# Optimization experiments

Measured on AMD Instinct MI355X. Metric: run time of the kernel, lower is better.

Reference implementation:

```python
import jax, jax.numpy as jnp
import numpy as np

N = 10000      # nodes
E = 160000     # edges (before self-loops)
IN = 256       # input feature dim
H = 8          # heads
C1, C2, C3 = 64, 128, 256  # per-head out channels per layer
NEG_SLOPE = 0.2


def setup_inputs() -> dict:
    key = jax.random.key(0)
    ks = jax.random.split(key, 16)
    def glorot(k, shape):
        fan_in = shape[-1]
        return jax.random.normal(k, shape, dtype=jnp.float32) * (1.0 / np.sqrt(fan_in))
    x = jax.random.normal(ks[0], (N, IN), dtype=jnp.float32)
    edge_index = jax.random.randint(ks[1], (2, E), 0, N)
    # layer 1: in=IN, out=64 per head, concat
    W1  = glorot(ks[2], (H * C1, IN))
    as1 = glorot(ks[3], (H, C1)); ad1 = glorot(ks[4], (H, C1))
    b1  = jnp.zeros((H * C1,), jnp.float32)
    # layer 2: in=H*C1, out=128 per head, concat
    W2  = glorot(ks[5], (H * C2, H * C1))
    as2 = glorot(ks[6], (H, C2)); ad2 = glorot(ks[7], (H, C2))
    b2  = jnp.zeros((H * C2,), jnp.float32)
    # layer 3: in=H*C2, out=256 per head, mean over heads
    W3  = glorot(ks[8], (H * C3, H * C2))
    as3 = glorot(ks[9], (H, C3)); ad3 = glorot(ks[10], (H, C3))
    b3  = jnp.zeros((C3,), jnp.float32)
    return {"x": x, "edge_index": edge_index,
            "W1": W1, "as1": as1, "ad1": ad1, "b1": b1,
            "W2": W2, "as2": as2, "ad2": ad2, "b2": b2,
            "W3": W3, "as3": as3, "ad3": ad3, "b3": b3}


def gat_layer(x, src, dst, W, a_src, a_dst, b, concat, num_nodes):
    """PyG-style GATConv (inference, dropout off, self-loops already in src/dst)."""
    heads, c = a_src.shape
    h = (x @ W.T).reshape(num_nodes, heads, c)          # [N,H,C]
    alpha_src = (h * a_src).sum(-1)                      # [N,H]
    alpha_dst = (h * a_dst).sum(-1)                      # [N,H]
    e = jax.nn.leaky_relu(alpha_src[src] + alpha_dst[dst], NEG_SLOPE)  # [E,H]
    # segment softmax over edges grouped by destination node
    m = jax.ops.segment_max(e, dst, num_segments=num_nodes)
    m = jnp.where(jnp.isfinite(m), m, 0.0)
    p = jnp.exp(e - m[dst])                              # [E,H]
    s = jax.ops.segment_sum(p, dst, num_segments=num_nodes)
    alpha = p / (s[dst] + 1e-16)                         # [E,H]
    out = jax.ops.segment_sum(alpha[:, :, None] * h[src], dst,
                              num_segments=num_nodes)    # [N,H,C]
    out = out.reshape(num_nodes, heads * c) if concat else out.mean(axis=1)
    return out + b


def reference(x, edge_index, W1, as1, ad1, b1, W2, as2, ad2, b2, W3, as3, ad3, b3):
    n = x.shape[0]
    loop = jnp.arange(n, dtype=edge_index.dtype)         # add_self_loops=True
    src = jnp.concatenate([edge_index[0], loop])
    dst = jnp.concatenate([edge_index[1], loop])
    h = jax.nn.elu(gat_layer(x, src, dst, W1, as1, ad1, b1, True, n))
    h = jax.nn.elu(gat_layer(h, src, dst, W2, as2, ad2, b2, True, n))
    return gat_layer(h, src, dst, W3, as3, ad3, b3, False, n)
```

## Files before the change

kernel.cpp:

```cpp
#include <hip/hip_runtime.h>
#include <cstdint>

#define NNODES 10000
#define NEDGES 160000
#define TOT_E  (NEDGES + NNODES)
#define HEADS  8

typedef unsigned short u16;
typedef __attribute__((ext_vector_type(8))) _Float16 h8;
typedef __attribute__((ext_vector_type(4))) _Float16 h4;
typedef __attribute__((ext_vector_type(4))) float f4;

__device__ inline u16 f2h(float x) {
    union { _Float16 h; u16 u; } c; c.h = (_Float16)x; return c.u;
}

__device__ inline void gld16(const u16* g, u16* l) {
    __builtin_amdgcn_global_load_lds(
        (const __attribute__((address_space(1))) void*)g,
        (__attribute__((address_space(3))) void*)l, 16, 0, 0);
}

__global__ void count_k(const int* __restrict__ ei, int* __restrict__ deg) {
    int i = blockIdx.x * 256 + threadIdx.x;
    if (i >= TOT_E) return;
    int dst = (i < NEDGES) ? ei[NEDGES + i] : (i - NEDGES);
    atomicAdd(deg + dst, 1);
}

__global__ __launch_bounds__(1024) void scan_k(const int* __restrict__ deg,
                                               int* __restrict__ rows) {
    __shared__ int buf[1024];
    int tid = threadIdx.x;
    int base = tid * 10;
    int loc[10]; int s = 0;
    #pragma unroll
    for (int j = 0; j < 10; j++) {
        int i = base + j;
        loc[j] = s;
        s += (i < NNODES) ? deg[i] : 0;
    }
    buf[tid] = s;
    __syncthreads();
    for (int off = 1; off < 1024; off <<= 1) {
        int t = (tid >= off) ? buf[tid - off] : 0;
        __syncthreads();
        buf[tid] += t;
        __syncthreads();
    }
    int ex = tid ? buf[tid - 1] : 0;
    #pragma unroll
    for (int j = 0; j < 10; j++) {
        int i = base + j;
        if (i < NNODES) rows[i] = ex + loc[j];
    }
    if (tid == 1023) rows[NNODES] = buf[1023];
}

__global__ void scatter_k(const int* __restrict__ ei, const int* __restrict__ rows,
                          int* __restrict__ cursor, int* __restrict__ esrc) {
    int i = blockIdx.x * 256 + threadIdx.x;
    if (i >= TOT_E) return;
    int src, dst;
    if (i < NEDGES) { src = ei[i]; dst = ei[NEDGES + i]; }
    else            { src = i - NEDGES; dst = src; }
    int pos = atomicAdd(cursor + dst, 1);
    esrc[rows[dst] + pos] = src;
}

__global__ void cvt16_k(const float* __restrict__ in, u16* __restrict__ o, int n4) {
    int i = blockIdx.x * 256 + threadIdx.x;
    if (i >= n4) return;
    float4 v = ((const float4*)in)[i];
    ushort4 h;
    h.x = f2h(v.x); h.y = f2h(v.y); h.z = f2h(v.z); h.w = f2h(v.w);
    ((ushort4*)o)[i] = h;
}

__global__ __launch_bounds__(256) void gemm_f16(
    const u16* __restrict__ A, const u16* __restrict__ B,
    u16* __restrict__ C16, int M, int N, int K,
    const float* __restrict__ a_s, const float* __restrict__ a_d,
    float* __restrict__ asrc, float* __restrict__ adst, int Chead)
{
    __shared__ u16 sA[4096], sB[4096];
    const int t = threadIdx.x, lane = t & 63, w = t >> 6;
    const int row0 = blockIdx.y * 128, col0 = blockIdx.x * 128;
    const int wm = w & 1, wn = w >> 1;
    const int l15 = lane & 15, quad = lane >> 4;

    const int octg = (lane & 3) ^ ((lane >> 3) & 3);
    const int rl   = lane >> 2;
    const u16* gp[4]; u16* lp[4];
    #pragma unroll
    for (int q = 0; q < 4; q++) {
        int c = w * 4 + q;
        if (c < 8) {
            int gr = row0 + c * 16 + rl; if (gr >= M) gr = M - 1;
            gp[q] = A + (size_t)gr * K + octg * 8;
            lp[q] = sA + c * 512;
        } else {
            int gc = col0 + (c - 8) * 16 + rl;
            gp[q] = B + (size_t)gc * K + octg * 8;
            lp[q] = sB + (c - 8) * 512;
        }
    }

    const int sw   = (l15 >> 1) & 3;
    const int aoff = (wm * 64 + l15) * 32 + ((quad ^ sw) * 8);
    const int boff = (wn * 64 + l15) * 32 + ((quad ^ sw) * 8);

    f4 acc[4][4];
    #pragma unroll
    for (int i = 0; i < 4; i++)
        #pragma unroll
        for (int j = 0; j < 4; j++)
            acc[i][j] = (f4){0.f, 0.f, 0.f, 0.f};

    for (int k0 = 0; k0 < K; k0 += 32) {
        #pragma unroll
        for (int q = 0; q < 4; q++) {
            gld16(gp[q], lp[q]);
            gp[q] += 32;
        }
        __syncthreads();

        h8 a[4];
        #pragma unroll
        for (int i = 0; i < 4; i++)
            a[i] = *(const h8*)&sA[aoff + i * 512];
        #pragma unroll
        for (int j = 0; j < 4; j++) {
            h8 b = *(const h8*)&sB[boff + j * 512];
            #pragma unroll
            for (int i = 0; i < 4; i++)
                acc[i][j] = __builtin_amdgcn_mfma_f32_16x16x32_f16(a[i], b, acc[i][j], 0, 0, 0);
        }
        __syncthreads();
    }

    const int span0 = col0 + wn * 64;
    const int hd = span0 / Chead;
    float av[4], dv[4];
    #pragma unroll
    for (int j = 0; j < 4; j++) {
        av[j] = a_s[span0 + j * 16 + l15];
        dv[j] = a_d[span0 + j * 16 + l15];
    }

    #pragma unroll
    for (int i = 0; i < 4; i++) {
        #pragma unroll
        for (int r = 0; r < 4; r++) {
            int gr = row0 + wm * 64 + i * 16 + quad * 4 + r;
            float s1 = 0.f, s2 = 0.f;
            #pragma unroll
            for (int j = 0; j < 4; j++) {
                float v = acc[i][j][r];
                s1 += v * av[j];
                s2 += v * dv[j];
            }
            #pragma unroll
            for (int m = 1; m < 16; m <<= 1) {
                s1 += __shfl_xor(s1, m);
                s2 += __shfl_xor(s2, m);
            }
            if (gr < M) {
                u16* cp = C16 + (size_t)gr * N + span0 + l15;
                #pragma unroll
                for (int j = 0; j < 4; j++)
                    cp[j * 16] = f2h(acc[i][j][r]);
                if (l15 == 0) {
                    atomicAdd(asrc + gr * HEADS + hd, s1);
                    atomicAdd(adst + gr * HEADS + hd, s2);
                }
            }
        }
    }
}

template<int C, int MODE>
__global__ __launch_bounds__(512) void agg_k(const u16* __restrict__ h16,
                                             const float* __restrict__ asrc,
                                             const float* __restrict__ adst,
                                             const int* __restrict__ rows,
                                             const int* __restrict__ esrc,
                                             const float* __restrict__ bias,
                                             u16* __restrict__ oh,
                                             float* __restrict__ outf) {
    constexpr int LPE = C / 4;
    constexpr int EPW = 64 / LPE;
    constexpr int U   = (LPE == 64) ? 16 : (LPE == 32) ? 12 : 8;
    __shared__ float red[MODE == 1 ? HEADS * 256 : 8];

    const int n    = blockIdx.x;
    const int hd   = threadIdx.x >> 6;
    const int lane = threadIdx.x & 63;
    const int sub  = lane / LPE;
    const int cl   = lane % LPE;
    const int beg = rows[n], end = rows[n + 1], deg = end - beg;
    const float ad = adst[n * HEADS + hd];

    float4 acc = {0.f, 0.f, 0.f, 0.f};

    auto gather = [&](int e, float pw, int cdeg) {
        for (int j = 0; j < cdeg; j += EPW * U) {
            int   sn[U]; float wg[U];
            #pragma unroll
            for (int u = 0; u < U; u++) {
                int idx = j + sub + EPW * u;
                int   ss = __shfl(e, idx);
                float ww = __shfl(pw, idx);
                bool ok = idx < cdeg;
                sn[u] = ok ? ss : 0;
                wg[u] = ok ? ww : 0.f;
            }
            h4 v[U];
            #pragma unroll
            for (int u = 0; u < U; u++)
                v[u] = *(const h4*)(h16 + (size_t)sn[u] * (HEADS * C) + hd * C + cl * 4);
            #pragma unroll
            for (int u = 0; u < U; u++) {
                acc.x += wg[u] * (float)v[u].x; acc.y += wg[u] * (float)v[u].y;
                acc.z += wg[u] * (float)v[u].z; acc.w += wg[u] * (float)v[u].w;
            }
        }
    };

    if (deg <= 64) {
        int e = 0; float p = 0.f;
        if (lane < deg) {
            e = esrc[beg + lane];
            float lg = asrc[e * HEADS + hd] + ad;
            lg = (lg > 0.f) ? lg : 0.2f * lg;
            p = __expf(lg);
        }
        float s = p;
        #pragma unroll
        for (int off = 32; off; off >>= 1) s += __shfl_xor(s, off);
        float pw = p / (s + 1e-16f);
        gather(e, pw, deg);
    } else {
        float ssum = 0.f;
        for (int i = beg + lane; i < end; i += 64) {
            float lg = asrc[esrc[i] * HEADS + hd] + ad;
            lg = (lg > 0.f) ? lg : 0.2f * lg;
            ssum += __expf(lg);
        }
        #pragma unroll
        for (int off = 32; off; off >>= 1) ssum += __shfl_xor(ssum, off);
        float inv = 1.f / (ssum + 1e-16f);
        for (int c0 = beg; c0 < end; c0 += 64) {
            int cdeg = min(64, end - c0);
            int e = 0; float pw = 0.f;
            if (lane < cdeg) {
                e = esrc[c0 + lane];
                float lg = asrc[e * HEADS + hd] + ad;
                lg = (lg > 0.f) ? lg : 0.2f * lg;
                pw = __expf(lg) * inv;
            }
            gather(e, pw, cdeg);
        }
    }

    #pragma unroll
    for (int m = LPE; m < 64; m <<= 1) {
        acc.x += __shfl_xor(acc.x, m); acc.y += __shfl_xor(acc.y, m);
        acc.z += __shfl_xor(acc.z, m); acc.w += __shfl_xor(acc.w, m);
    }

    if constexpr (MODE == 0) {
        if (sub == 0) {
            const float* bp = bias + hd * C + cl * 4;
            float4 b = *(const float4*)bp;
            float r[4] = {acc.x + b.x, acc.y + b.y, acc.z + b.z, acc.w + b.w};
            #pragma unroll
            for (int j = 0; j < 4; j++)
                r[j] = (r[j] > 0.f) ? r[j] : (expf(r[j]) - 1.f);
            ushort4 hv;
            hv.x = f2h(r[0]); hv.y = f2h(r[1]); hv.z = f2h(r[2]); hv.w = f2h(r[3]);
            *(ushort4*)(oh + (size_t)n * (HEADS * C) + hd * C + cl * 4) = hv;
        }
    } else {
        *(float4*)&red[hd * 256 + lane * 4] = acc;
        __syncthreads();
        int tid = threadIdx.x;
        if (tid < 256) {
            float s = 0.f;
            #pragma unroll
            for (int hh = 0; hh < HEADS; hh++) s += red[hh * 256 + tid];
            outf[(size_t)n * 256 + tid] = s * 0.125f + bias[tid];
        }
    }
}

extern "C" void kernel_launch(void* const* d_in, const int* in_sizes, int n_in,
                              void* d_out, int out_size, void* d_ws, size_t ws_size,
                              hipStream_t stream) {
    const float* x   = (const float*)d_in[0];
    const int*   ei  = (const int*)d_in[1];
    const float* W1  = (const float*)d_in[2];
    const float* as1 = (const float*)d_in[3];
    const float* ad1 = (const float*)d_in[4];
    const float* b1  = (const float*)d_in[5];
    const float* W2  = (const float*)d_in[6];
    const float* as2 = (const float*)d_in[7];
    const float* ad2 = (const float*)d_in[8];
    const float* b2  = (const float*)d_in[9];
    const float* W3  = (const float*)d_in[10];
    const float* as3 = (const float*)d_in[11];
    const float* ad3 = (const float*)d_in[12];
    const float* b3  = (const float*)d_in[13];
    float* out = (float*)d_out;

    int* deg    = (int*)d_ws;
    int* cursor = deg + 10240;
    int* rows   = cursor + 10240;
    int* esrc   = rows + 10240;
    float* asrc = (float*)(esrc + 170240);
    float* adst = asrc + 81920;
    u16* Hh     = (u16*)(adst + 81920);
    u16* Af     = Hh + (size_t)NNODES * 2048;
    u16* Wf     = Af + (size_t)NNODES * 1024;

    hipMemsetAsync(deg, 0, 2 * 10240 * sizeof(int), stream);

    count_k<<<(TOT_E + 255) / 256, 256, 0, stream>>>(ei, deg);
    scan_k<<<1, 1024, 0, stream>>>(deg, rows);
    scatter_k<<<(TOT_E + 255) / 256, 256, 0, stream>>>(ei, rows, cursor, esrc);

    const int rowBlocks = (NNODES + 127) / 128;

    cvt16_k<<<(NNODES * 256 / 4 + 255) / 256, 256, 0, stream>>>(x, Af, NNODES * 256 / 4);
    cvt16_k<<<(512 * 256 / 4 + 255) / 256, 256, 0, stream>>>(W1, Wf, 512 * 256 / 4);
    hipMemsetAsync(asrc, 0, 2 * 81920 * sizeof(float), stream);
    gemm_f16<<<dim3(4, rowBlocks), 256, 0, stream>>>(Af, Wf, Hh, NNODES, 512, 256,
                                                     as1, ad1, asrc, adst, 64);
    agg_k<64, 0><<<NNODES, 512, 0, stream>>>(Hh, asrc, adst, rows, esrc, b1, Af, nullptr);

    cvt16_k<<<(1024 * 512 / 4 + 255) / 256, 256, 0, stream>>>(W2, Wf, 1024 * 512 / 4);
    hipMemsetAsync(asrc, 0, 2 * 81920 * sizeof(float), stream);
    gemm_f16<<<dim3(8, rowBlocks), 256, 0, stream>>>(Af, Wf, Hh, NNODES, 1024, 512,
                                                     as2, ad2, asrc, adst, 128);
    agg_k<128, 0><<<NNODES, 512, 0, stream>>>(Hh, asrc, adst, rows, esrc, b2, Af, nullptr);

    cvt16_k<<<(2048 * 1024 / 4 + 255) / 256, 256, 0, stream>>>(W3, Wf, 2048 * 1024 / 4);
    hipMemsetAsync(asrc, 0, 2 * 81920 * sizeof(float), stream);
    gemm_f16<<<dim3(16, rowBlocks), 256, 0, stream>>>(Af, Wf, Hh, NNODES, 2048, 1024,
                                                      as3, ad3, asrc, adst, 256);
    agg_k<256, 1><<<NNODES, 512, 0, stream>>>(Hh, asrc, adst, rows, esrc, b3, nullptr, out);
}
```

Measured before the change: 483.0 us.

## Double-buffer GEMM LDS loads and widen layer-3 aggregation gathers to 8 halves

The GEMM now keeps two LDS buffers and issues the global-to-LDS loads for the next K tile before computing the current one. It uses explicit vmcnt waits and raw barriers so memory latency overlaps with MFMA work. Separately, the C=256 aggregation path loads 8 fp16 values per lane instead of 4, so each edge needs half the lanes and two edges are processed per wavefront pass. This raises register use per lane and makes the GEMM's correctness depend on the hand-written waitcnt encoding.

```diff
diff --git a/kernel.cpp b/kernel.cpp
--- a/kernel.cpp
+++ b/kernel.cpp
@@ -10,6 +10,8 @@
 typedef __attribute__((ext_vector_type(8))) _Float16 h8;
 typedef __attribute__((ext_vector_type(4))) _Float16 h4;
 typedef __attribute__((ext_vector_type(4))) float f4;
+
+#define WAIT_VM(n) __builtin_amdgcn_s_waitcnt(0x0F70 | (n))
 
 __device__ inline u16 f2h(float x) {
     union { _Float16 h; u16 u; } c; c.h = (_Float16)x; return c.u;
@@ -83,7 +85,7 @@
     const float* __restrict__ a_s, const float* __restrict__ a_d,
     float* __restrict__ asrc, float* __restrict__ adst, int Chead)
 {
-    __shared__ u16 sA[4096], sB[4096];
+    __shared__ u16 sh[2][8192];
     const int t = threadIdx.x, lane = t & 63, w = t >> 6;
     const int row0 = blockIdx.y * 128, col0 = blockIdx.x * 128;
     const int wm = w & 1, wn = w >> 1;
@@ -91,24 +93,25 @@
 
     const int octg = (lane & 3) ^ ((lane >> 3) & 3);
     const int rl   = lane >> 2;
-    const u16* gp[4]; u16* lp[4];
+    const u16* gp[4]; int lofs[4];
     #pragma unroll
     for (int q = 0; q < 4; q++) {
         int c = w * 4 + q;
         if (c < 8) {
             int gr = row0 + c * 16 + rl; if (gr >= M) gr = M - 1;
             gp[q] = A + (size_t)gr * K + octg * 8;
-            lp[q] = sA + c * 512;
+            lofs[q] = c * 512;
         } else {
             int gc = col0 + (c - 8) * 16 + rl;
             gp[q] = B + (size_t)gc * K + octg * 8;
-            lp[q] = sB + (c - 8) * 512;
-        }
-    }
-
-    const int sw   = (l15 >> 1) & 3;
-    const int aoff = (wm * 64 + l15) * 32 + ((quad ^ sw) * 8);
-    const int boff = (wn * 64 + l15) * 32 + ((quad ^ sw) * 8);
+            lofs[q] = 4096 + (c - 8) * 512;
+        }
+    }
+
+    const int sw = (l15 >> 1) & 3;
+    const int po = (quad ^ sw) * 8;
+    const int arow = (wm * 64 + l15) * 32;
+    const int brow = 4096 + (wn * 64 + l15) * 32;
 
     f4 acc[4][4];
     #pragma unroll
@@ -117,26 +120,35 @@
         for (int j = 0; j < 4; j++)
             acc[i][j] = (f4){0.f, 0.f, 0.f, 0.f};
 
-    for (int k0 = 0; k0 < K; k0 += 32) {
-        #pragma unroll
-        for (int q = 0; q < 4; q++) {
-            gld16(gp[q], lp[q]);
-            gp[q] += 32;
-        }
-        __syncthreads();
-
+    const int T = K >> 5;
+
+    #pragma unroll
+    for (int q = 0; q < 4; q++) { gld16(gp[q], &sh[0][lofs[q]]); gp[q] += 32; }
+
+    for (int k = 0; k < T; k++) {
+        const int p = k & 1;
+        if (k + 1 < T) {
+            #pragma unroll
+            for (int q = 0; q < 4; q++) { gld16(gp[q], &sh[1 - p][lofs[q]]); gp[q] += 32; }
+            WAIT_VM(4);
+        } else {
+            WAIT_VM(0);
+        }
+        __builtin_amdgcn_s_barrier();
+
+        const u16* sa = &sh[p][0];
         h8 a[4];
         #pragma unroll
         for (int i = 0; i < 4; i++)
-            a[i] = *(const h8*)&sA[aoff + i * 512];
+            a[i] = *(const h8*)&sa[arow + i * 512 + po];
         #pragma unroll
         for (int j = 0; j < 4; j++) {
-            h8 b = *(const h8*)&sB[boff + j * 512];
+            h8 b = *(const h8*)&sa[brow + j * 512 + po];
             #pragma unroll
             for (int i = 0; i < 4; i++)
                 acc[i][j] = __builtin_amdgcn_mfma_f32_16x16x32_f16(a[i], b, acc[i][j], 0, 0, 0);
         }
-        __syncthreads();
+        __builtin_amdgcn_s_barrier();
     }
 
     const int span0 = col0 + wn * 64;
@@ -188,9 +200,10 @@
                                              const float* __restrict__ bias,
                                              u16* __restrict__ oh,
                                              float* __restrict__ outf) {
-    constexpr int LPE = C / 4;
+    constexpr int VEC = (C == 256) ? 8 : 4;
+    constexpr int LPE = C / VEC;
     constexpr int EPW = 64 / LPE;
-    constexpr int U   = (LPE == 64) ? 16 : (LPE == 32) ? 12 : 8;
+    constexpr int U   = (VEC == 8) ? 8 : ((LPE == 32) ? 12 : 8);
     __shared__ float red[MODE == 1 ? HEADS * 256 : 8];
 
     const int n    = blockIdx.x;
@@ -201,7 +214,7 @@
     const int beg = rows[n], end = rows[n + 1], deg = end - beg;
     const float ad = adst[n * HEADS + hd];
 
-    float4 acc = {0.f, 0.f, 0.f, 0.f};
+    float acc[VEC] = {};
 
     auto gather = [&](int e, float pw, int cdeg) {
         for (int j = 0; j < cdeg; j += EPW * U) {
@@ -215,14 +228,26 @@
                 sn[u] = ok ? ss : 0;
                 wg[u] = ok ? ww : 0.f;
             }
-            h4 v[U];
-            #pragma unroll
-            for (int u = 0; u < U; u++)
-                v[u] = *(const h4*)(h16 + (size_t)sn[u] * (HEADS * C) + hd * C + cl * 4);
-            #pragma unroll
-            for (int u = 0; u < U; u++) {
-                acc.x += wg[u] * (float)v[u].x; acc.y += wg[u] * (float)v[u].y;
-                acc.z += wg[u] * (float)v[u].z; acc.w += wg[u] * (float)v[u].w;
+            if constexpr (VEC == 8) {
+                h8 v[U];
+                #pragma unroll
+                for (int u = 0; u < U; u++)
+                    v[u] = *(const h8*)(h16 + (size_t)sn[u] * (HEADS * C) + hd * C + cl * 8);
+                #pragma unroll
+                for (int u = 0; u < U; u++)
+                    #pragma unroll
+                    for (int i = 0; i < 8; i++)
+                        acc[i] += wg[u] * (float)v[u][i];
+            } else {
+                h4 v[U];
+                #pragma unroll
+                for (int u = 0; u < U; u++)
+                    v[u] = *(const h4*)(h16 + (size_t)sn[u] * (HEADS * C) + hd * C + cl * 4);
+                #pragma unroll
+                for (int u = 0; u < U; u++)
+                    #pragma unroll
+                    for (int i = 0; i < 4; i++)
+                        acc[i] += wg[u] * (float)v[u][i];
             }
         }
     };
@@ -264,16 +289,16 @@
     }
 
     #pragma unroll
-    for (int m = LPE; m < 64; m <<= 1) {
-        acc.x += __shfl_xor(acc.x, m); acc.y += __shfl_xor(acc.y, m);
-        acc.z += __shfl_xor(acc.z, m); acc.w += __shfl_xor(acc.w, m);
-    }
+    for (int m = LPE; m < 64; m <<= 1)
+        #pragma unroll
+        for (int i = 0; i < VEC; i++)
+            acc[i] += __shfl_xor(acc[i], m);
 
     if constexpr (MODE == 0) {
         if (sub == 0) {
             const float* bp = bias + hd * C + cl * 4;
             float4 b = *(const float4*)bp;
-            float r[4] = {acc.x + b.x, acc.y + b.y, acc.z + b.z, acc.w + b.w};
+            float r[4] = {acc[0] + b.x, acc[1] + b.y, acc[2] + b.z, acc[3] + b.w};
             #pragma unroll
             for (int j = 0; j < 4; j++)
                 r[j] = (r[j] > 0.f) ? r[j] : (expf(r[j]) - 1.f);
@@ -282,7 +307,12 @@
             *(ushort4*)(oh + (size_t)n * (HEADS * C) + hd * C + cl * 4) = hv;
         }
     } else {
-        *(float4*)&red[hd * 256 + lane * 4] = acc;
+        if (sub == 0) {
+            float4 v0{acc[0], acc[1], acc[2], acc[3]};
+            float4 v1{acc[4], acc[5], acc[6], acc[7]};
+            *(float4*)&red[hd * 256 + cl * 8]     = v0;
+            *(float4*)&red[hd * 256 + cl * 8 + 4] = v1;
+        }
         __syncthreads();
         int tid = threadIdx.x;
         if (tid < 256) {
```

After: 469.2 us. 2.9% less time.

## Triple-buffer GEMM shared-memory tiles with async global-to-LDS prefetch

Applied to the files above, without the earlier changes.

Replaces the single-buffer K loop in the f16 MFMA GEMM with a three-stage LDS ring buffer. Global-to-LDS loads for tile k+2 are issued before computing tile k, and explicit vmcnt waits plus raw barriers replace __syncthreads. This is meant to hide global memory latency behind MFMA work, at the cost of three times the LDS footprint (48KB per block), which may reduce occupancy.

```diff
diff --git a/kernel.cpp b/kernel.cpp
--- a/kernel.cpp
+++ b/kernel.cpp
@@ -10,6 +10,8 @@
 typedef __attribute__((ext_vector_type(8))) _Float16 h8;
 typedef __attribute__((ext_vector_type(4))) _Float16 h4;
 typedef __attribute__((ext_vector_type(4))) float f4;
+
+#define WAIT_VM(n) __builtin_amdgcn_s_waitcnt(0x0F70 | (n))
 
 __device__ inline u16 f2h(float x) {
     union { _Float16 h; u16 u; } c; c.h = (_Float16)x; return c.u;
@@ -83,7 +85,7 @@
     const float* __restrict__ a_s, const float* __restrict__ a_d,
     float* __restrict__ asrc, float* __restrict__ adst, int Chead)
 {
-    __shared__ u16 sA[4096], sB[4096];
+    __shared__ u16 sh[3][8192];
     const int t = threadIdx.x, lane = t & 63, w = t >> 6;
     const int row0 = blockIdx.y * 128, col0 = blockIdx.x * 128;
     const int wm = w & 1, wn = w >> 1;
@@ -91,24 +93,25 @@
 
     const int octg = (lane & 3) ^ ((lane >> 3) & 3);
     const int rl   = lane >> 2;
-    const u16* gp[4]; u16* lp[4];
+    const u16* gp[4]; int lofs[4];
     #pragma unroll
     for (int q = 0; q < 4; q++) {
         int c = w * 4 + q;
         if (c < 8) {
             int gr = row0 + c * 16 + rl; if (gr >= M) gr = M - 1;
             gp[q] = A + (size_t)gr * K + octg * 8;
-            lp[q] = sA + c * 512;
+            lofs[q] = c * 512;
         } else {
             int gc = col0 + (c - 8) * 16 + rl;
             gp[q] = B + (size_t)gc * K + octg * 8;
-            lp[q] = sB + (c - 8) * 512;
-        }
-    }
-
-    const int sw   = (l15 >> 1) & 3;
-    const int aoff = (wm * 64 + l15) * 32 + ((quad ^ sw) * 8);
-    const int boff = (wn * 64 + l15) * 32 + ((quad ^ sw) * 8);
+            lofs[q] = 4096 + (c - 8) * 512;
+        }
+    }
+
+    const int sw = (l15 >> 1) & 3;
+    const int po = (quad ^ sw) * 8;
+    const int arow = (wm * 64 + l15) * 32;
+    const int brow = 4096 + (wn * 64 + l15) * 32;
 
     f4 acc[4][4];
     #pragma unroll
@@ -117,26 +120,39 @@
         for (int j = 0; j < 4; j++)
             acc[i][j] = (f4){0.f, 0.f, 0.f, 0.f};
 
-    for (int k0 = 0; k0 < K; k0 += 32) {
-        #pragma unroll
-        for (int q = 0; q < 4; q++) {
-            gld16(gp[q], lp[q]);
-            gp[q] += 32;
-        }
-        __syncthreads();
-
+    const int T = K >> 5;
+
+    #pragma unroll
+    for (int q = 0; q < 4; q++) { gld16(gp[q], &sh[0][lofs[q]]); gp[q] += 32; }
+    #pragma unroll
+    for (int q = 0; q < 4; q++) { gld16(gp[q], &sh[1][lofs[q]]); gp[q] += 32; }
+
+    for (int k = 0; k < T; k++) {
+        if (k + 2 < T) {
+            u16* dst = &sh[(k + 2) % 3][0];
+            #pragma unroll
+            for (int q = 0; q < 4; q++) { gld16(gp[q], dst + lofs[q]); gp[q] += 32; }
+            WAIT_VM(8);
+        } else if (k + 2 == T) {
+            WAIT_VM(4);
+        } else {
+            WAIT_VM(0);
+        }
+        __builtin_amdgcn_s_barrier();
+
+        const u16* sa = &sh[k % 3][0];
         h8 a[4];
         #pragma unroll
         for (int i = 0; i < 4; i++)
-            a[i] = *(const h8*)&sA[aoff + i * 512];
+            a[i] = *(const h8*)&sa[arow + i * 512 + po];
         #pragma unroll
         for (int j = 0; j < 4; j++) {
-            h8 b = *(const h8*)&sB[boff + j * 512];
+            h8 b = *(const h8*)&sa[brow + j * 512 + po];
             #pragma unroll
             for (int i = 0; i < 4; i++)
                 acc[i][j] = __builtin_amdgcn_mfma_f32_16x16x32_f16(a[i], b, acc[i][j], 0, 0, 0);
         }
-        __syncthreads();
+        __builtin_amdgcn_s_barrier();
     }
 
     const int span0 = col0 + wn * 64;
```

Result: faster. 466.1 us (-3.5%).
